# Optimization experiments

Hardware: AMD Instinct MI355X
Metric: run time of the kernel (lower is better)

The kernel has to match this reference:

```python
import jax, jax.numpy as jnp
import numpy as np

LN_EPS = 1e-5


def setup_inputs() -> dict:
    key = jax.random.key(0)
    ks = jax.random.split(key, 5)
    B, I, H = 16384, 512, 512
    x = jax.random.normal(ks[0], (B, I), dtype=jnp.float32)
    h_prev = jax.random.normal(ks[1], (B, H), dtype=jnp.float32)
    c_prev = jax.random.normal(ks[2], (B, H), dtype=jnp.float32)
    # torch nn.Linear weight layout: [out_features, in_features]
    W = jax.random.normal(ks[3], (4 * H, I + H), dtype=jnp.float32) * (1.0 / np.sqrt(I + H))
    b = jnp.zeros((4 * H,), dtype=jnp.float32)
    gamma = jnp.ones((H,), dtype=jnp.float32)
    beta = jnp.zeros((H,), dtype=jnp.float32)
    Wp = jax.random.normal(ks[4], (H, H), dtype=jnp.float32) * (1.0 / np.sqrt(H))
    return {"x": x, "h_prev": h_prev, "c_prev": c_prev, "W": W, "b": b,
            "gamma": gamma, "beta": beta, "Wp": Wp}


def _layernorm(c, gamma, beta):
    mu = jnp.mean(c, axis=-1, keepdims=True)
    var = jnp.mean(jnp.square(c - mu), axis=-1, keepdims=True)
    return (c - mu) * jax.lax.rsqrt(var + LN_EPS) * gamma + beta


def reference(x, h_prev, c_prev, W, b, gamma, beta, Wp):
    # combined: [B, I+H]; gates: [B, 4H]
    combined = jnp.concatenate([x, h_prev], axis=1)
    gates = combined @ W.T + b
    i, f, g, o = jnp.split(gates, 4, axis=1)
    i = jax.nn.sigmoid(i)
    f = jax.nn.sigmoid(f)
    g = jnp.tanh(g)
    o = jax.nn.sigmoid(o)
    cell = f * c_prev + i * g
    cell = _layernorm(cell, gamma, beta)
    out = (o * jnp.tanh(cell)) @ Wp.T  # projection, no bias
    return (out, cell)
```

## Files before the change

### kernel.cpp

```cpp
#include <hip/hip_runtime.h>
#include <hip/hip_bf16.h>


typedef __attribute__((ext_vector_type(4))) float f32x4;
typedef __attribute__((ext_vector_type(8))) short bf16x8;
typedef __attribute__((ext_vector_type(4))) short bf16x4;

#define NB 16384
#define NH 512

__device__ __forceinline__ short f2bf(float f) {
    union { float f; unsigned u; } v; v.f = f;
    unsigned r = v.u + 0x7FFFu + ((v.u >> 16) & 1u);
    return (short)(r >> 16);
}
__device__ __forceinline__ float bf2f(short s) {
    union { unsigned u; float f; } v; v.u = ((unsigned)(unsigned short)s) << 16;
    return v.f;
}
__device__ __forceinline__ float sigmoidf_(float x) { return 1.0f / (1.0f + __expf(-x)); }
__device__ __forceinline__ float tanhf_(float x) { return 1.0f - 2.0f / (__expf(2.0f * x) + 1.0f); }

__device__ __forceinline__ void gld16(const void* g, void* l) {
    __builtin_amdgcn_global_load_lds(
        (const __attribute__((address_space(1))) void*)g,
        (__attribute__((address_space(3))) void*)l, 16, 0, 0);
}

__global__ __launch_bounds__(256, 8)
void k_convert(const float* __restrict__ x, const float* __restrict__ h,
               const float* __restrict__ W, const float* __restrict__ Wp,
               short* __restrict__ Abf, short* __restrict__ Wbf,
               short* __restrict__ Wpbf)
{
    const long long nA  = (long long)NB * 256;
    const long long nW  = (long long)2048 * 1024 / 4;
    const long long nWp = (long long)512 * 512 / 4;
    long long i = (long long)blockIdx.x * 256 + threadIdx.x;
    const long long stride = (long long)gridDim.x * 256;
    for (; i < nA + nW + nWp; i += stride) {
        const float* src; short* dst;
        if (i < nA) {
            const int r  = (int)(i >> 8);
            const int c4 = (int)(i & 255);
            src = (c4 < 128) ? (x + (size_t)r * 512 + c4 * 4)
                             : (h + (size_t)r * 512 + (c4 - 128) * 4);
            dst = Abf + i * 4;
        } else if (i < nA + nW) {
            const long long j = i - nA;
            src = W + j * 4; dst = Wbf + j * 4;
        } else {
            const long long j = i - nA - nW;
            src = Wp + j * 4; dst = Wpbf + j * 4;
        }
        f32x4 v = *(const f32x4*)src;
        bf16x4 o;
#pragma unroll
        for (int j = 0; j < 4; ++j) o[j] = f2bf(v[j]);
        *(bf16x4*)dst = o;
    }
}

__global__ __launch_bounds__(256, 4)
void k_gates_cell(const short* __restrict__ Abf, const short* __restrict__ Wbf,
                  const float* __restrict__ c_prev, const float* __restrict__ bvec,
                  float* __restrict__ cell_raw, short* __restrict__ o_ws)
{
    __shared__ __align__(16) short As[128 * 64];
    __shared__ __align__(16) short Bs[128 * 64];

    const int tid  = threadIdx.x;
    const int lane = tid & 63;
    const int wid  = tid >> 6;
    const int wr = wid >> 1, wc = wid & 1;
    const int row0 = blockIdx.x * 128;
    const int h0   = blockIdx.y * 32;

    const f32x4 zero = {0.f, 0.f, 0.f, 0.f};
    f32x4 acc[4][4];
#pragma unroll
    for (int m = 0; m < 4; ++m)
#pragma unroll
        for (int n = 0; n < 4; ++n) acc[m][n] = zero;

    const int k8 = ((lane & 7) ^ (lane >> 3)) * 8;
    int aOff[4], bOff[4];
#pragma unroll
    for (int j = 0; j < 4; ++j) {
        const int row = (wid * 4 + j) * 8 + (lane >> 3);
        aOff[j] = (row0 + row) * 1024 + k8;
        const int gate = (row >> 4) & 3;
        const int wrow = gate * 512 + h0 + (row >> 6) * 16 + (row & 15);
        bOff[j] = wrow * 1024 + k8;
    }

    for (int kt = 0; kt < 16; ++kt) {
        const int kbase = kt * 64;
#pragma unroll
        for (int j = 0; j < 4; ++j) {
            gld16(Abf + aOff[j] + kbase, As + (wid * 4 + j) * 512);
            gld16(Wbf + bOff[j] + kbase, Bs + (wid * 4 + j) * 512);
        }
        __syncthreads();
#pragma unroll
        for (int kk = 0; kk < 64; kk += 32) {
            bf16x8 af[4], bfr[4];
#pragma unroll
            for (int m = 0; m < 4; ++m) {
                const int row = wr * 64 + m * 16 + (lane & 15);
                int byt = row * 128 + (kk + (lane >> 4) * 8) * 2;
                byt ^= (row & 7) << 4;
                af[m] = *(const bf16x8*)((const char*)As + byt);
            }
#pragma unroll
            for (int n = 0; n < 4; ++n) {
                const int row = wc * 64 + n * 16 + (lane & 15);
                int byt = row * 128 + (kk + (lane >> 4) * 8) * 2;
                byt ^= (row & 7) << 4;
                bfr[n] = *(const bf16x8*)((const char*)Bs + byt);
            }
#pragma unroll
            for (int m = 0; m < 4; ++m)
#pragma unroll
                for (int n = 0; n < 4; ++n)
                    acc[m][n] = __builtin_amdgcn_mfma_f32_16x16x32_bf16(af[m], bfr[n], acc[m][n], 0, 0, 0);
        }
        __syncthreads();
    }

    const int hcol = h0 + wc * 16 + (lane & 15);
    float bias[4];
#pragma unroll
    for (int n = 0; n < 4; ++n) bias[n] = bvec[n * 512 + hcol];
#pragma unroll
    for (int m = 0; m < 4; ++m) {
        const int rbase = row0 + wr * 64 + m * 16 + ((lane >> 4) * 4);
#pragma unroll
        for (int q = 0; q < 4; ++q) {
            const size_t idx = (size_t)(rbase + q) * 512 + hcol;
            const float iv = acc[m][0][q] + bias[0];
            const float fv = acc[m][1][q] + bias[1];
            const float gv = acc[m][2][q] + bias[2];
            const float ov = acc[m][3][q] + bias[3];
            const float c = c_prev[idx];
            cell_raw[idx] = sigmoidf_(fv) * c + sigmoidf_(iv) * tanhf_(gv);
            o_ws[idx] = f2bf(sigmoidf_(ov));
        }
    }
}

__global__ __launch_bounds__(256)
void k_layernorm(const float* __restrict__ gamma, const float* __restrict__ beta,
                 float* __restrict__ cell, short* __restrict__ s_io)
{
    const int r = blockIdx.x * 4 + (threadIdx.x >> 6);
    const int lane = threadIdx.x & 63;
    float* row = cell + (size_t)r * 512;
    f32x4 v0 = *(const f32x4*)(row + lane * 8);
    f32x4 v1 = *(const f32x4*)(row + lane * 8 + 4);
    float s1 = 0.f, s2 = 0.f;
#pragma unroll
    for (int j = 0; j < 4; ++j) {
        s1 += v0[j] + v1[j];
        s2 += v0[j] * v0[j] + v1[j] * v1[j];
    }
#pragma unroll
    for (int off = 32; off > 0; off >>= 1) {
        s1 += __shfl_xor(s1, off);
        s2 += __shfl_xor(s2, off);
    }
    const float mu  = s1 * (1.f / 512.f);
    const float var = s2 * (1.f / 512.f) - mu * mu;
    const float rs  = rsqrtf(var + 1e-5f);
    const f32x4 g0 = *(const f32x4*)(gamma + lane * 8);
    const f32x4 g1 = *(const f32x4*)(gamma + lane * 8 + 4);
    const f32x4 b0 = *(const f32x4*)(beta + lane * 8);
    const f32x4 b1 = *(const f32x4*)(beta + lane * 8 + 4);
    const bf16x8 o8 = *(const bf16x8*)(s_io + (size_t)r * 512 + lane * 8);
    f32x4 c0, c1; bf16x8 s8;
#pragma unroll
    for (int j = 0; j < 4; ++j) {
        c0[j] = (v0[j] - mu) * rs * g0[j] + b0[j];
        c1[j] = (v1[j] - mu) * rs * g1[j] + b1[j];
    }
#pragma unroll
    for (int j = 0; j < 4; ++j) {
        s8[j]     = f2bf(bf2f(o8[j])     * tanhf_(c0[j]));
        s8[j + 4] = f2bf(bf2f(o8[j + 4]) * tanhf_(c1[j]));
    }
    *(f32x4*)(row + lane * 8)     = c0;
    *(f32x4*)(row + lane * 8 + 4) = c1;
    *(bf16x8*)(s_io + (size_t)r * 512 + lane * 8) = s8;
}

__global__ __launch_bounds__(256, 4)
void k_proj(const short* __restrict__ s_ws, const short* __restrict__ Wpbf,
            float* __restrict__ out)
{
    __shared__ __align__(16) short As[128 * 64];
    __shared__ __align__(16) short Bs[128 * 64];
    const int tid = threadIdx.x;
    const int lane = tid & 63;
    const int wid = tid >> 6;
    const int wr = wid >> 1, wc = wid & 1;
    const int row0 = blockIdx.x * 128;
    const int col0 = blockIdx.y * 128;

    const f32x4 zero = {0.f, 0.f, 0.f, 0.f};
    f32x4 acc[4][4];
#pragma unroll
    for (int m = 0; m < 4; ++m)
#pragma unroll
        for (int n = 0; n < 4; ++n) acc[m][n] = zero;

    const int k8 = ((lane & 7) ^ (lane >> 3)) * 8;
    int aOff[4], bOff[4];
#pragma unroll
    for (int j = 0; j < 4; ++j) {
        const int row = (wid * 4 + j) * 8 + (lane >> 3);
        aOff[j] = (row0 + row) * 512 + k8;
        bOff[j] = (col0 + row) * 512 + k8;
    }

    for (int kt = 0; kt < 8; ++kt) {
        const int kbase = kt * 64;
#pragma unroll
        for (int j = 0; j < 4; ++j) {
            gld16(s_ws + aOff[j] + kbase, As + (wid * 4 + j) * 512);
            gld16(Wpbf + bOff[j] + kbase, Bs + (wid * 4 + j) * 512);
        }
        __syncthreads();
#pragma unroll
        for (int kk = 0; kk < 64; kk += 32) {
            bf16x8 af[4], bfr[4];
#pragma unroll
            for (int m = 0; m < 4; ++m) {
                const int row = wr * 64 + m * 16 + (lane & 15);
                int byt = row * 128 + (kk + (lane >> 4) * 8) * 2;
                byt ^= (row & 7) << 4;
                af[m] = *(const bf16x8*)((const char*)As + byt);
            }
#pragma unroll
            for (int n = 0; n < 4; ++n) {
                const int row = wc * 64 + n * 16 + (lane & 15);
                int byt = row * 128 + (kk + (lane >> 4) * 8) * 2;
                byt ^= (row & 7) << 4;
                bfr[n] = *(const bf16x8*)((const char*)Bs + byt);
            }
#pragma unroll
            for (int m = 0; m < 4; ++m)
#pragma unroll
                for (int n = 0; n < 4; ++n)
                    acc[m][n] = __builtin_amdgcn_mfma_f32_16x16x32_bf16(af[m], bfr[n], acc[m][n], 0, 0, 0);
        }
        __syncthreads();
    }

#pragma unroll
    for (int m = 0; m < 4; ++m) {
        const int grow = row0 + wr * 64 + m * 16 + ((lane >> 4) * 4);
#pragma unroll
        for (int n = 0; n < 4; ++n) {
            const int gcol = col0 + wc * 64 + n * 16 + (lane & 15);
#pragma unroll
            for (int q = 0; q < 4; ++q)
                out[(size_t)(grow + q) * 512 + gcol] = acc[m][n][q];
        }
    }
}

extern "C" void kernel_launch(void* const* d_in, const int* in_sizes, int n_in,
                              void* d_out, int out_size, void* d_ws, size_t ws_size,
                              hipStream_t stream) {
    (void)in_sizes; (void)n_in; (void)out_size; (void)ws_size;
    const float* x      = (const float*)d_in[0];
    const float* h_prev = (const float*)d_in[1];
    const float* c_prev = (const float*)d_in[2];
    const float* W      = (const float*)d_in[3];
    const float* bvec   = (const float*)d_in[4];
    const float* gamma  = (const float*)d_in[5];
    const float* beta   = (const float*)d_in[6];
    const float* Wp     = (const float*)d_in[7];

    float* out  = (float*)d_out;
    float* cell = out + (size_t)NB * NH;
    short* Abf  = (short*)d_out;
    short* s_io = (short*)d_ws;
    short* Wbf  = s_io + (size_t)NB * NH;
    short* Wpbf = Wbf + (size_t)2048 * 1024;

    k_convert<<<2048, 256, 0, stream>>>(x, h_prev, W, Wp, Abf, Wbf, Wpbf);
    dim3 g1(NB / 128, 2048 / 128);
    k_gates_cell<<<g1, 256, 0, stream>>>(Abf, Wbf, c_prev, bvec, cell, s_io);
    k_layernorm<<<NB / 4, 256, 0, stream>>>(gamma, beta, cell, s_io);
    dim3 g3(NB / 128, NH / 128);
    k_proj<<<g3, 256, 0, stream>>>(s_io, Wpbf, out);
}
```

Measured before the change: 258.3 us.

## Enlarge gates GEMM tile to 256x256 with double-buffered LDS pipeline

Result: slower. 292.5 us (+13.3%).

```diff
diff --git a/kernel.cpp b/kernel.cpp
--- a/kernel.cpp
+++ b/kernel.cpp
@@ -61,87 +61,126 @@
     }
 }
 
-__global__ __launch_bounds__(256, 4)
+__global__ __launch_bounds__(512, 2)
 void k_gates_cell(const short* __restrict__ Abf, const short* __restrict__ Wbf,
                   const float* __restrict__ c_prev, const float* __restrict__ bvec,
                   float* __restrict__ cell_raw, short* __restrict__ o_ws)
 {
-    __shared__ __align__(16) short As[128 * 64];
-    __shared__ __align__(16) short Bs[128 * 64];
+    __shared__ __align__(16) short As[2][256 * 64];
+    __shared__ __align__(16) short Bs[2][256 * 64];
 
     const int tid  = threadIdx.x;
     const int lane = tid & 63;
-    const int wid  = tid >> 6;
-    const int wr = wid >> 1, wc = wid & 1;
-    const int row0 = blockIdx.x * 128;
-    const int h0   = blockIdx.y * 32;
+    const int w    = tid >> 6;
+    const int wr = w >> 2, wc = w & 3;
+    const int row0 = blockIdx.x * 256;
+    const int h0   = blockIdx.y * 64;
 
     const f32x4 zero = {0.f, 0.f, 0.f, 0.f};
-    f32x4 acc[4][4];
-#pragma unroll
-    for (int m = 0; m < 4; ++m)
+    f32x4 acc[8][4];
+#pragma unroll
+    for (int m = 0; m < 8; ++m)
 #pragma unroll
         for (int n = 0; n < 4; ++n) acc[m][n] = zero;
 
-    const int k8 = ((lane & 7) ^ (lane >> 3)) * 8;
-    int aOff[4], bOff[4];
-#pragma unroll
-    for (int j = 0; j < 4; ++j) {
-        const int row = (wid * 4 + j) * 8 + (lane >> 3);
-        aOff[j] = (row0 + row) * 1024 + k8;
-        const int gate = (row >> 4) & 3;
-        const int wrow = gate * 512 + h0 + (row >> 6) * 16 + (row & 15);
-        bOff[j] = wrow * 1024 + k8;
-    }
-
-    for (int kt = 0; kt < 16; ++kt) {
-        const int kbase = kt * 64;
-#pragma unroll
-        for (int j = 0; j < 4; ++j) {
-            gld16(Abf + aOff[j] + kbase, As + (wid * 4 + j) * 512);
-            gld16(Wbf + bOff[j] + kbase, Bs + (wid * 4 + j) * 512);
-        }
-        __syncthreads();
-#pragma unroll
-        for (int kk = 0; kk < 64; kk += 32) {
-            bf16x8 af[4], bfr[4];
-#pragma unroll
-            for (int m = 0; m < 4; ++m) {
-                const int row = wr * 64 + m * 16 + (lane & 15);
-                int byt = row * 128 + (kk + (lane >> 4) * 8) * 2;
-                byt ^= (row & 7) << 4;
-                af[m] = *(const bf16x8*)((const char*)As + byt);
-            }
-#pragma unroll
-            for (int n = 0; n < 4; ++n) {
-                const int row = wc * 64 + n * 16 + (lane & 15);
-                int byt = row * 128 + (kk + (lane >> 4) * 8) * 2;
-                byt ^= (row & 7) << 4;
-                bfr[n] = *(const bf16x8*)((const char*)Bs + byt);
-            }
-#pragma unroll
-            for (int m = 0; m < 4; ++m)
-#pragma unroll
-                for (int n = 0; n < 4; ++n)
-                    acc[m][n] = __builtin_amdgcn_mfma_f32_16x16x32_bf16(af[m], bfr[n], acc[m][n], 0, 0, 0);
-        }
-        __syncthreads();
-    }
+    const int srcK8 = ((tid & 7) ^ ((tid >> 3) & 7)) * 8;
+    int aOff[4], bOff[4], ldsB[4];
+#pragma unroll
+    for (int j = 0; j < 4; ++j) {
+        const int row = j * 64 + (tid >> 3);
+        aOff[j] = (row0 + row) * 1024 + srcK8;
+        const int wrow = ((row >> 4) & 3) * 512 + h0 + (row >> 6) * 16 + (row & 15);
+        bOff[j] = wrow * 1024 + srcK8;
+        ldsB[j] = (j * 512 + w * 64) * 8;
+    }
+
+#define STAGE(tile, buf) do {                                          \
+        const int kb_ = (tile) * 64;                                   \
+        _Pragma("unroll")                                              \
+        for (int j_ = 0; j_ < 4; ++j_) {                               \
+            gld16(Abf + aOff[j_] + kb_, &As[(buf)][ldsB[j_]]);         \
+            gld16(Wbf + bOff[j_] + kb_, &Bs[(buf)][ldsB[j_]]);         \
+        }                                                              \
+    } while (0)
+
+#define COMPUTE(buf) do {                                              \
+        _Pragma("unroll")                                              \
+        for (int q_ = 0; q_ < 4; ++q_) {                               \
+            const int g_ = q_ >> 1, kk_ = (q_ & 1) * 32;               \
+            bf16x8 af[4], bfr[4];                                      \
+            _Pragma("unroll")                                          \
+            for (int mi_ = 0; mi_ < 4; ++mi_) {                        \
+                const int row_ = wr * 128 + (g_ * 4 + mi_) * 16 + (lane & 15); \
+                int byt_ = row_ * 128 + (kk_ + (lane >> 4) * 8) * 2;   \
+                byt_ ^= (row_ & 7) << 4;                               \
+                af[mi_] = *(const bf16x8*)((const char*)As[(buf)] + byt_); \
+            }                                                          \
+            _Pragma("unroll")                                          \
+            for (int n_ = 0; n_ < 4; ++n_) {                           \
+                const int row_ = wc * 64 + n_ * 16 + (lane & 15);      \
+                int byt_ = row_ * 128 + (kk_ + (lane >> 4) * 8) * 2;   \
+                byt_ ^= (row_ & 7) << 4;                               \
+                bfr[n_] = *(const bf16x8*)((const char*)Bs[(buf)] + byt_); \
+            }                                                          \
+            __builtin_amdgcn_s_setprio(1);                             \
+            _Pragma("unroll")                                          \
+            for (int mi_ = 0; mi_ < 4; ++mi_)                          \
+                _Pragma("unroll")                                      \
+                for (int n_ = 0; n_ < 4; ++n_)                         \
+                    acc[g_ * 4 + mi_][n_] = __builtin_amdgcn_mfma_f32_16x16x32_bf16( \
+                        af[mi_], bfr[n_], acc[g_ * 4 + mi_][n_], 0, 0, 0); \
+            __builtin_amdgcn_s_setprio(0);                             \
+        }                                                              \
+    } while (0)
+
+    STAGE(0, 0);
+    STAGE(1, 1);
+    asm volatile("s_waitcnt vmcnt(8)" ::: "memory");
+    __builtin_amdgcn_s_barrier();
+
+#pragma unroll 1
+    for (int t = 0; t < 16; t += 2) {
+        COMPUTE(0);
+        asm volatile("s_waitcnt lgkmcnt(0)" ::: "memory");
+        __builtin_amdgcn_sched_barrier(0);
+        __builtin_amdgcn_s_barrier();
+        if (t + 2 < 16) {
+            STAGE(t + 2, 0);
+            asm volatile("s_waitcnt vmcnt(8)" ::: "memory");
+        } else {
+            asm volatile("s_waitcnt vmcnt(0)" ::: "memory");
+        }
+        __builtin_amdgcn_s_barrier();
+
+        COMPUTE(1);
+        asm volatile("s_waitcnt lgkmcnt(0)" ::: "memory");
+        __builtin_amdgcn_sched_barrier(0);
+        __builtin_amdgcn_s_barrier();
+        if (t + 3 < 16) {
+            STAGE(t + 3, 1);
+            asm volatile("s_waitcnt vmcnt(8)" ::: "memory");
+        } else {
+            asm volatile("s_waitcnt vmcnt(0)" ::: "memory");
+        }
+        __builtin_amdgcn_s_barrier();
+    }
+#undef STAGE
+#undef COMPUTE
 
     const int hcol = h0 + wc * 16 + (lane & 15);
     float bias[4];
 #pragma unroll
     for (int n = 0; n < 4; ++n) bias[n] = bvec[n * 512 + hcol];
 #pragma unroll
-    for (int m = 0; m < 4; ++m) {
-        const int rbase = row0 + wr * 64 + m * 16 + ((lane >> 4) * 4);
+    for (int mi = 0; mi < 8; ++mi) {
+        const int rbase = row0 + wr * 128 + mi * 16 + ((lane >> 4) * 4);
 #pragma unroll
         for (int q = 0; q < 4; ++q) {
             const size_t idx = (size_t)(rbase + q) * 512 + hcol;
-            const float iv = acc[m][0][q] + bias[0];
-            const float fv = acc[m][1][q] + bias[1];
-            const float gv = acc[m][2][q] + bias[2];
-            const float ov = acc[m][3][q] + bias[3];
+            const float iv = acc[mi][0][q] + bias[0];
+            const float fv = acc[mi][1][q] + bias[1];
+            const float gv = acc[mi][2][q] + bias[2];
+            const float ov = acc[mi][3][q] + bias[3];
             const float c = c_prev[idx];
             cell_raw[idx] = sigmoidf_(fv) * c + sigmoidf_(iv) * tanhf_(gv);
             o_ws[idx] = f2bf(sigmoidf_(ov));
@@ -290,8 +329,8 @@
     short* Wpbf = Wbf + (size_t)2048 * 1024;
 
     k_convert<<<2048, 256, 0, stream>>>(x, h_prev, W, Wp, Abf, Wbf, Wpbf);
-    dim3 g1(NB / 128, 2048 / 128);
-    k_gates_cell<<<g1, 256, 0, stream>>>(Abf, Wbf, c_prev, bvec, cell, s_io);
+    dim3 g1(NB / 256, 2048 / 256);
+    k_gates_cell<<<g1, 512, 0, stream>>>(Abf, Wbf, c_prev, bvec, cell, s_io);
     k_layernorm<<<NB / 4, 256, 0, stream>>>(gamma, beta, cell, s_io);
     dim3 g3(NB / 128, NH / 128);
     k_proj<<<g3, 256, 0, stream>>>(s_io, Wpbf, out);
```
